# Kernel optimization log

Measured on AMD Instinct MI355X. Metric: run time of the kernel, lower is better.

The kernel has to match this reference:

```python
import jax, jax.numpy as jnp
import numpy as np

B, T, D = 4, 2048, 2048
N_HEADS, N_KV = 16, 4
HEAD_DIM = D // N_HEADS  # 128
N_REP = N_HEADS // N_KV
THETA = 10000.0


def _rope_cos_sin(seq_len, dim, theta):
    inv_freq = 1.0 / (theta ** (jnp.arange(0, dim, 2, dtype=jnp.float32) / dim))
    t = jnp.arange(seq_len, dtype=jnp.float32)
    freqs = jnp.outer(t, inv_freq)               # [T, dim/2]
    emb = jnp.concatenate([freqs, freqs], -1)    # [T, dim]
    return jnp.cos(emb)[None, None], jnp.sin(emb)[None, None]  # [1,1,T,dim]


def _rotate_half(x):
    x1, x2 = jnp.split(x, 2, axis=-1)
    return jnp.concatenate([-x2, x1], axis=-1)


def setup_inputs() -> dict:
    key = jax.random.key(0)
    ks = jax.random.split(key, 5)
    x = jax.random.normal(ks[0], (B, T, D), dtype=jnp.float32)
    # additive causal mask
    causal = jnp.tril(jnp.ones((T, T), dtype=bool))
    mask = jnp.where(causal, 0.0, -1e9).astype(jnp.float32)[None, None]
    s = 0.02
    wq = jax.random.normal(ks[1], (D, N_HEADS * HEAD_DIM), dtype=jnp.float32) * s
    wk = jax.random.normal(ks[2], (D, N_KV * HEAD_DIM), dtype=jnp.float32) * s
    wv = jax.random.normal(ks[3], (D, N_KV * HEAD_DIM), dtype=jnp.float32) * s
    wo = jax.random.normal(ks[4], (D, D), dtype=jnp.float32) * s
    return {"x": x, "mask": mask, "wq": wq, "wk": wk, "wv": wv, "wo": wo}


def reference(x, mask, wq, wk, wv, wo):
    Bc, Tc, _ = x.shape
    q = (x @ wq).reshape(Bc, Tc, N_HEADS, HEAD_DIM).transpose(0, 2, 1, 3)  # [B,H,T,hd]
    k = (x @ wk).reshape(Bc, Tc, N_KV, HEAD_DIM).transpose(0, 2, 1, 3)     # [B,Kv,T,hd]
    v = (x @ wv).reshape(Bc, Tc, N_KV, HEAD_DIM).transpose(0, 2, 1, 3)

    cos, sin = _rope_cos_sin(Tc, HEAD_DIM, THETA)
    q = q * cos + _rotate_half(q) * sin
    k = k * cos + _rotate_half(k) * sin

    # repeat kv heads: [B,Kv,T,hd] -> [B,Kv*n_rep,T,hd]
    k = jnp.repeat(k, N_REP, axis=1)
    v = jnp.repeat(v, N_REP, axis=1)

    scale = HEAD_DIM ** -0.5
    attn = jnp.einsum("bhqd,bhkd->bhqk", q, k) * scale
    attn = attn + mask
    attn = jax.nn.softmax(attn, axis=-1)
    out = jnp.einsum("bhqk,bhkd->bhqd", attn, v)  # [B,H,T,hd]
    out = out.transpose(0, 2, 1, 3).reshape(Bc, Tc, -1)
    return out @ wo
```

## Files before the change

kernel.cpp:

```cpp
#include <hip/hip_runtime.h>

typedef __bf16 bf16;
typedef float  f32x4  __attribute__((ext_vector_type(4)));
typedef float  f32x2  __attribute__((ext_vector_type(2)));
typedef float  f32x16 __attribute__((ext_vector_type(16)));
typedef __bf16 bf16x8 __attribute__((ext_vector_type(8)));
typedef __bf16 bf16x4 __attribute__((ext_vector_type(4)));
typedef unsigned short ushort4_ __attribute__((ext_vector_type(4)));
typedef unsigned int   uint2_   __attribute__((ext_vector_type(2)));

typedef unsigned int __attribute__((address_space(1))) uint_g;
typedef unsigned int __attribute__((address_space(3))) uint_l;

#define DEV __device__ __forceinline__

DEV void gload16(const void* g, void* l) {
  __builtin_amdgcn_global_load_lds((uint_g*)g, (uint_l*)l, 16, 0, 0);
}

#define PHASE_SYNC do { \
  asm volatile("s_barrier" ::: "memory"); \
  asm volatile("s_waitcnt lgkmcnt(0)" ::: "memory"); \
  __builtin_amdgcn_sched_barrier(0); } while (0)

__global__ void k_cvt(const float* __restrict__ in, bf16* __restrict__ out) {
  int i = blockIdx.x * 256 + threadIdx.x;
  f32x4 v = *((const f32x4*)in + i);
  bf16x4 o;
  o[0] = (bf16)v[0]; o[1] = (bf16)v[1]; o[2] = (bf16)v[2]; o[3] = (bf16)v[3];
  *((bf16x4*)out + i) = o;
}

__global__ void k_transpose_cvt(const float* __restrict__ in, bf16* __restrict__ out,
                                int K, int N) {
  __shared__ bf16 tile[64][65];
  int n0 = blockIdx.x * 64, k0 = blockIdx.y * 64;
  int tx = threadIdx.x & 63, ty = threadIdx.x >> 6;
#pragma unroll
  for (int r = 0; r < 64; r += 4)
    tile[r + ty][tx] = (bf16)in[(size_t)(k0 + r + ty) * N + n0 + tx];
  __syncthreads();
#pragma unroll
  for (int r = 0; r < 64; r += 4)
    out[(size_t)(n0 + r + ty) * K + k0 + tx] = tile[tx][r + ty];
}

__global__ void k_rope_tab(f32x2* __restrict__ tab) {
  int idx = blockIdx.x * 256 + threadIdx.x;
  int t = idx >> 6, i = idx & 63;
  float inv = powf(10000.f, -(float)i * (1.f / 64.f));
  float ang = (float)t * inv;
  f32x2 cs; cs[0] = cosf(ang); cs[1] = sinf(ang);
  tab[idx] = cs;
}

template <int MODE>
__global__ __launch_bounds__(512, 2) void k_gemm256(const bf16* __restrict__ A,
                                                    const bf16* __restrict__ Bt,
                                                    void* __restrict__ Cq,
                                                    bf16* __restrict__ Ck,
                                                    bf16* __restrict__ Cv,
                                                    int K) {
  __shared__ bf16 Asm[2][256 * 64];
  __shared__ bf16 Bsm[2][256 * 64];
  const int tid = threadIdx.x;
  const int w = tid >> 6, l = tid & 63, lr = l & 15, lg = l >> 4;
  const int wr = w >> 2, wc = w & 3;
  const int bn = blockIdx.x, bm = blockIdx.y;

  const int srow = tid >> 3;
  const int scb = ((tid & 7) << 4) ^ ((srow & 7) << 4);
  const bf16* Ag = A  + ((size_t)(bm * 256) + srow) * K;
  const bf16* Bg = Bt + ((size_t)(bn * 256) + srow) * K;
  const int ldsbase = w << 10;

  auto stA = [&](int buf, int s, int k0) {
    gload16((const char*)Ag + ((size_t)(s * 64) * K + k0) * 2 + scb,
            (char*)&Asm[buf][0] + s * 8192 + ldsbase);
  };
  auto stB = [&](int buf, int s, int k0) {
    gload16((const char*)Bg + ((size_t)(s * 64) * K + k0) * 2 + scb,
            (char*)&Bsm[buf][0] + s * 8192 + ldsbase);
  };
  auto ldA = [&](int buf, int mf, int kk) -> bf16x8 {
    int row = wr * 128 + mf * 16 + lr;
    return *(const bf16x8*)((const char*)&Asm[buf][0] + row * 128 +
                            ((kk * 64 + lg * 16) ^ ((lr & 7) << 4)));
  };
  auto ldB = [&](int buf, int nf, int kk) -> bf16x8 {
    int row = wc * 64 + nf * 16 + lr;
    return *(const bf16x8*)((const char*)&Bsm[buf][0] + row * 128 +
                            ((kk * 64 + lg * 16) ^ ((lr & 7) << 4)));
  };

  f32x4 acc[8][4] = {};
  const int nt = K >> 6;

#pragma unroll
  for (int s = 0; s < 4; s++) { stA(0, s, 0); stB(0, s, 0); }
  asm volatile("s_waitcnt vmcnt(0)" ::: "memory");
  __syncthreads();

#pragma unroll 1
  for (int t = 0; t < nt; t++) {
    const int cur = t & 1, nxt = cur ^ 1;
    const int kn = (t + 1) << 6;
    const bool pre = (t + 1 < nt);
    bf16x8 a0[4][2], a1[4][2], b0[2][2], b1[2][2];

#pragma unroll
    for (int mf = 0; mf < 4; mf++) { a0[mf][0] = ldA(cur, mf, 0); a0[mf][1] = ldA(cur, mf, 1); }
#pragma unroll
    for (int nf = 0; nf < 2; nf++) { b0[nf][0] = ldB(cur, nf, 0); b0[nf][1] = ldB(cur, nf, 1); }
    if (pre) { stA(nxt, 0, kn); stA(nxt, 1, kn); stA(nxt, 2, kn); }
    PHASE_SYNC;
    __builtin_amdgcn_s_setprio(1);
#pragma unroll
    for (int mf = 0; mf < 4; mf++)
#pragma unroll
      for (int nf = 0; nf < 2; nf++)
#pragma unroll
        for (int kk = 0; kk < 2; kk++)
          acc[mf][nf] = __builtin_amdgcn_mfma_f32_16x16x32_bf16(a0[mf][kk], b0[nf][kk], acc[mf][nf], 0, 0, 0);
    __builtin_amdgcn_s_setprio(0);

#pragma unroll
    for (int nf = 0; nf < 2; nf++) { b1[nf][0] = ldB(cur, nf + 2, 0); b1[nf][1] = ldB(cur, nf + 2, 1); }
    if (pre) { stA(nxt, 3, kn); stB(nxt, 0, kn); stB(nxt, 1, kn); }
    PHASE_SYNC;
    __builtin_amdgcn_s_setprio(1);
#pragma unroll
    for (int mf = 0; mf < 4; mf++)
#pragma unroll
      for (int nf = 0; nf < 2; nf++)
#pragma unroll
        for (int kk = 0; kk < 2; kk++)
          acc[mf][nf + 2] = __builtin_amdgcn_mfma_f32_16x16x32_bf16(a0[mf][kk], b1[nf][kk], acc[mf][nf + 2], 0, 0, 0);
    __builtin_amdgcn_s_setprio(0);

#pragma unroll
    for (int mf = 0; mf < 4; mf++) { a1[mf][0] = ldA(cur, mf + 4, 0); a1[mf][1] = ldA(cur, mf + 4, 1); }
#pragma unroll
    for (int nf = 0; nf < 2; nf++) { b0[nf][0] = ldB(cur, nf, 0); b0[nf][1] = ldB(cur, nf, 1); }
    if (pre) { stB(nxt, 2, kn); stB(nxt, 3, kn); }
    PHASE_SYNC;
    __builtin_amdgcn_s_setprio(1);
#pragma unroll
    for (int mf = 0; mf < 4; mf++)
#pragma unroll
      for (int nf = 0; nf < 2; nf++)
#pragma unroll
        for (int kk = 0; kk < 2; kk++)
          acc[mf + 4][nf] = __builtin_amdgcn_mfma_f32_16x16x32_bf16(a1[mf][kk], b0[nf][kk], acc[mf + 4][nf], 0, 0, 0);
    __builtin_amdgcn_s_setprio(0);

    __builtin_amdgcn_s_setprio(1);
#pragma unroll
    for (int mf = 0; mf < 4; mf++)
#pragma unroll
      for (int nf = 0; nf < 2; nf++)
#pragma unroll
        for (int kk = 0; kk < 2; kk++)
          acc[mf + 4][nf + 2] = __builtin_amdgcn_mfma_f32_16x16x32_bf16(a1[mf][kk], b1[nf][kk], acc[mf + 4][nf + 2], 0, 0, 0);
    __builtin_amdgcn_s_setprio(0);
    asm volatile("s_waitcnt vmcnt(0)" ::: "memory");
    asm volatile("s_barrier" ::: "memory");
  }

#pragma unroll
  for (int mf = 0; mf < 8; mf++) {
    const int rowb = bm * 256 + wr * 128 + mf * 16 + lg * 4;
#pragma unroll
    for (int nf = 0; nf < 4; nf++) {
      const int col = bn * 256 + wc * 64 + nf * 16 + lr;
      if constexpr (MODE == 0) {
        float* Cf = (float*)Cq;
#pragma unroll
        for (int j = 0; j < 4; j++)
          Cf[(size_t)(rowb + j) * 2048 + col] = acc[mf][nf][j];
      } else {
        if (bn < 8) {
          bf16* Cb = (bf16*)Cq;
#pragma unroll
          for (int j = 0; j < 4; j++)
            Cb[(size_t)(rowb + j) * 2048 + col] = (bf16)acc[mf][nf][j];
        } else if (bn < 10) {
          int kcol = col - 2048;
#pragma unroll
          for (int j = 0; j < 4; j++)
            Ck[(size_t)(rowb + j) * 512 + kcol] = (bf16)acc[mf][nf][j];
        } else {
          int vcol = col - 2560;
          int kv = vcol >> 7, d = vcol & 127;
          int bb = rowb >> 11, t0 = rowb & 2047;
          size_t off = ((size_t)((bb * 4 + kv) * 128 + d)) * 2048 + t0;
          ushort4_ pk;
#pragma unroll
          for (int j = 0; j < 4; j++)
            pk[j] = __builtin_bit_cast(unsigned short, (bf16)acc[mf][nf][j]);
          *(ushort4_*)(Cv + off) = pk;
        }
      }
    }
  }
}

template <int LOGNH>
__global__ void k_rope(const bf16* __restrict__ in, bf16* __restrict__ out,
                       const f32x2* __restrict__ tab, float scl) {
  const int NH = 1 << LOGNH;
  int idx = blockIdx.x * 256 + threadIdx.x;
  int dq = idx & 15;
  int h = (idx >> 4) & (NH - 1);
  int bt = idx >> (4 + LOGNH);
  int t = bt & 2047;
  int d0 = dq * 4;
  const bf16* pin = in + (size_t)bt * (NH * 128) + h * 128;
  bf16x4 x1 = *(const bf16x4*)(pin + d0);
  bf16x4 x2 = *(const bf16x4*)(pin + 64 + d0);
  bf16x4 o1, o2;
#pragma unroll
  for (int j = 0; j < 4; j++) {
    f32x2 cs = tab[t * 64 + d0 + j];
    float c1 = cs[0] * scl, s1 = cs[1] * scl;
    float a = (float)x1[j], c2 = (float)x2[j];
    o1[j] = (bf16)(a * c1 - c2 * s1);
    o2[j] = (bf16)(c2 * c1 + a * s1);
  }
  int b = bt >> 11;
  bf16* pout = out + (((size_t)(b << LOGNH) + h) * 2048 + t) * 128;
  *(bf16x4*)(pout + d0) = o1;
  *(bf16x4*)(pout + 64 + d0) = o2;
}

__global__ __launch_bounds__(256, 2) void k_attn(const bf16* __restrict__ Qb,
                                                 const bf16* __restrict__ Kb,
                                                 const bf16* __restrict__ Vt,
                                                 bf16* __restrict__ AO) {
  __shared__ bf16 Ks[2][64 * 128];
  __shared__ bf16 Vs[2][128 * 64];
  __shared__ bf16 Ps[4][32 * 64];
  const int tid = threadIdx.x, w = tid >> 6, l = tid & 63;
  const int bh = blockIdx.y, b = bh >> 4, h = bh & 15, kvh = h >> 2;
  const int pi = blockIdx.x;
  const int l31 = l & 31, hi = l >> 5;

  const bf16* Kh = Kb + (size_t)(b * 4 + kvh) * (2048 * 128);
  const bf16* Vh = Vt + (size_t)(b * 4 + kvh) * (128 * 2048);
  char* Pw = (char*)&Ps[w][0] + l31 * 128;
  const int qsw = (l & 7) << 4;

  auto stage = [&](int kv0, int buf) {
#pragma unroll
    for (int i = 0; i < 4; i++) {
      int krow = w * 16 + i * 4 + (l >> 4);
      int kcb = ((l & 15) * 16) ^ ((krow & 7) << 4);
      gload16(Kh + (size_t)(kv0 + krow) * 128 + (kcb >> 1), (bf16*)&Ks[buf][0] + w * 2048 + i * 512);
      int vrow = w * 32 + i * 8 + (l >> 3);
      int vcb = ((l & 7) * 16) ^ ((vrow & 7) << 4);
      gload16(Vh + (size_t)vrow * 2048 + kv0 + (vcb >> 1), (bf16*)&Vs[buf][0] + w * 2048 + i * 512);
    }
  };

#pragma unroll 1
  for (int ph = 0; ph < 2; ph++) {
    const int q0 = (ph ? (15 - pi) : pi) * 128;
    const int nt = q0 / 64 + 2;
    const int qw0 = q0 + w * 32;
    const int qg = qw0 + l31;

    bf16x8 qf[8];
    {
      const bf16* qp = Qb + (((size_t)(b * 16 + h) * 2048) + qg) * 128 + hi * 8;
#pragma unroll
      for (int kk = 0; kk < 8; kk++) qf[kk] = *(const bf16x8*)(qp + kk * 16);
    }

    f32x16 ot[4] = {};
    float m_ = -3e38f, l_ = 0.f;

    int cur = 0;
    stage(0, 0);
    __syncthreads();

#pragma unroll 1
    for (int t = 0; t < nt; t++) {
      const int kv0 = t * 64;
      if (t + 1 < nt) stage(kv0 + 64, cur ^ 1);

      if (kv0 <= qw0 + 31) {
        f32x16 st[2] = {};
        __builtin_amdgcn_s_setprio(1);
#pragma unroll
        for (int nb = 0; nb < 2; nb++) {
          const int row = nb * 32 + l31;
          const char* kbase = (const char*)&Ks[cur][0] + row * 256;
#pragma unroll
          for (int kk = 0; kk < 8; kk++) {
            bf16x8 kf = *(const bf16x8*)(kbase + ((kk * 32 + hi * 16) ^ qsw));
            st[nb] = __builtin_amdgcn_mfma_f32_32x32x16_bf16(kf, qf[kk], st[nb], 0, 0, 0);
          }
        }
        __builtin_amdgcn_s_setprio(0);

        if (kv0 + 63 > qw0) {
#pragma unroll
          for (int nb = 0; nb < 2; nb++) {
            const int kvb = kv0 + nb * 32 + 4 * hi;
#pragma unroll
            for (int r = 0; r < 16; r++) {
              int kg = kvb + (r & 3) + 8 * (r >> 2);
              if (kg > qg) st[nb][r] = -3e38f;
            }
          }
        }
        float mx = -3e38f;
#pragma unroll
        for (int nb = 0; nb < 2; nb++)
#pragma unroll
          for (int r = 0; r < 16; r++) mx = fmaxf(mx, st[nb][r]);
        mx = fmaxf(mx, __shfl_xor(mx, 32));
        if (!__all(mx - m_ <= 8.f)) {
          float mnew = fmaxf(m_, mx);
          float corr = exp2f(m_ - mnew);
          m_ = mnew; l_ *= corr;
#pragma unroll
          for (int dt = 0; dt < 4; dt++)
#pragma unroll
            for (int r = 0; r < 16; r++) ot[dt][r] *= corr;
        }
        float ls = 0.f;
#pragma unroll
        for (int nb = 0; nb < 2; nb++)
#pragma unroll
          for (int a = 0; a < 4; a++) {
            uint2_ pr;
#pragma unroll
            for (int half = 0; half < 2; half++) {
              float p0 = exp2f(st[nb][4 * a + 2 * half] - m_);
              float p1 = exp2f(st[nb][4 * a + 2 * half + 1] - m_);
              ls += p0 + p1;
              unsigned short b0 = __builtin_bit_cast(unsigned short, (bf16)p0);
              unsigned short b1 = __builtin_bit_cast(unsigned short, (bf16)p1);
              pr[half] = (unsigned int)b0 | ((unsigned int)b1 << 16);
            }
            *(uint2_*)(Pw + ((nb * 64 + a * 16 + hi * 8) ^ qsw)) = pr;
          }
        ls += __shfl_xor(ls, 32);
        l_ += ls;

        __builtin_amdgcn_s_setprio(1);
#pragma unroll
        for (int kb = 0; kb < 4; kb++) {
          bf16x8 pb = *(const bf16x8*)(Pw + ((kb * 32 + hi * 16) ^ qsw));
#pragma unroll
          for (int dt = 0; dt < 4; dt++) {
            const int vrow = dt * 32 + l31;
            const char* vp = (const char*)&Vs[cur][0] + vrow * 128 + ((kb * 32 + hi * 16) ^ qsw);
            bf16x8 vf = *(const bf16x8*)vp;
            ot[dt] = __builtin_amdgcn_mfma_f32_32x32x16_bf16(vf, pb, ot[dt], 0, 0, 0);
          }
        }
        __builtin_amdgcn_s_setprio(0);
      }

      __syncthreads();
      cur ^= 1;
    }

    const float inv = 1.f / l_;
    bf16* op = AO + ((size_t)b * 2048 + qg) * 2048 + h * 128;
#pragma unroll
    for (int dt = 0; dt < 4; dt++)
#pragma unroll
      for (int rq = 0; rq < 4; rq++) {
        ushort4_ pk;
#pragma unroll
        for (int j = 0; j < 4; j++)
          pk[j] = __builtin_bit_cast(unsigned short, (bf16)(ot[dt][rq * 4 + j] * inv));
        *(ushort4_*)(op + dt * 32 + rq * 8 + hi * 4) = pk;
      }
  }
}

extern "C" void kernel_launch(void* const* d_in, const int* in_sizes, int n_in,
                              void* d_out, int out_size, void* d_ws, size_t ws_size,
                              hipStream_t stream) {
  const float* x  = (const float*)d_in[0];
  const float* wq = (const float*)d_in[2];
  const float* wk = (const float*)d_in[3];
  const float* wv = (const float*)d_in[4];
  const float* wo = (const float*)d_in[5];

  char* p = (char*)d_ws;
  auto alloc = [&](size_t bytes) { char* r = p; p += (bytes + 255) & ~(size_t)255; return r; };
  bf16*  xb     = (bf16*)alloc(8192ull * 2048 * 2);
  bf16*  wqkvT  = (bf16*)alloc(3072ull * 2048 * 2);
  bf16*  woT    = (bf16*)alloc(2048ull * 2048 * 2);
  f32x2* tab    = (f32x2*)alloc(2048ull * 64 * 8);
  bf16*  Qtmp   = (bf16*)alloc(8192ull * 2048 * 2);
  bf16*  Ktmp   = (bf16*)alloc(8192ull * 512 * 2);
  bf16*  Qr     = (bf16*)alloc(8192ull * 2048 * 2);
  bf16*  Kr     = (bf16*)alloc(8192ull * 512 * 2);
  bf16*  Vr     = (bf16*)alloc(8192ull * 512 * 2);

  k_cvt<<<16384, 256, 0, stream>>>(x, xb);
  k_transpose_cvt<<<dim3(32, 32), 256, 0, stream>>>(wq, wqkvT, 2048, 2048);
  k_transpose_cvt<<<dim3(8, 32),  256, 0, stream>>>(wk, wqkvT + 2048ull * 2048, 2048, 512);
  k_transpose_cvt<<<dim3(8, 32),  256, 0, stream>>>(wv, wqkvT + 2560ull * 2048, 2048, 512);
  k_transpose_cvt<<<dim3(32, 32), 256, 0, stream>>>(wo, woT, 2048, 2048);
  k_rope_tab<<<512, 256, 0, stream>>>(tab);

  k_gemm256<1><<<dim3(12, 32), 512, 0, stream>>>(xb, wqkvT, Qtmp, Ktmp, Vr, 2048);

  const float qscl = 0.08838834764831845f * 1.4426950408889634f;
  k_rope<4><<<8192, 256, 0, stream>>>(Qtmp, Qr, tab, qscl);
  k_rope<2><<<2048, 256, 0, stream>>>(Ktmp, Kr, tab, 1.0f);

  k_attn<<<dim3(8, 64), 256, 0, stream>>>(Qr, Kr, Vr, Qtmp);

  k_gemm256<0><<<dim3(8, 32), 512, 0, stream>>>(Qtmp, woT, d_out, nullptr, nullptr, 2048);
}
```

Baseline: 349.4 us.

## Reorder GEMM prefetch stages with finer barriers and partial vmcnt waits

Reworks the double-buffered bf16 GEMM main loop so the next tile's B stages are issued first and the A stages are spread across later phases. Each MFMA block now gets its own s_barrier, and the end-of-iteration full vmcnt(0) drain becomes partial vmcnt waits so some global-to-LDS loads stay in flight. The explicit lgkmcnt waits and sched_barrier are dropped, and launch bounds go from two blocks per CU to one, which frees registers. The risk is a hazard: if a read of the current buffer depends on an A stage still covered by a partial wait, results could be wrong, and the extra barriers add sync cost.

```diff
diff --git a/kernel.cpp b/kernel.cpp
--- a/kernel.cpp
+++ b/kernel.cpp
@@ -18,10 +18,8 @@
   __builtin_amdgcn_global_load_lds((uint_g*)g, (uint_l*)l, 16, 0, 0);
 }
 
-#define PHASE_SYNC do { \
-  asm volatile("s_barrier" ::: "memory"); \
-  asm volatile("s_waitcnt lgkmcnt(0)" ::: "memory"); \
-  __builtin_amdgcn_sched_barrier(0); } while (0)
+#define SBAR  asm volatile("s_barrier" ::: "memory")
+#define VMCNT(n) asm volatile("s_waitcnt vmcnt(" #n ")" ::: "memory")
 
 __global__ void k_cvt(const float* __restrict__ in, bf16* __restrict__ out) {
   int i = blockIdx.x * 256 + threadIdx.x;
@@ -55,7 +53,7 @@
 }
 
 template <int MODE>
-__global__ __launch_bounds__(512, 2) void k_gemm256(const bf16* __restrict__ A,
+__global__ __launch_bounds__(512, 1) void k_gemm256(const bf16* __restrict__ A,
                                                     const bf16* __restrict__ Bt,
                                                     void* __restrict__ Cq,
                                                     bf16* __restrict__ Ck,
@@ -98,8 +96,8 @@
 
 #pragma unroll
   for (int s = 0; s < 4; s++) { stA(0, s, 0); stB(0, s, 0); }
-  asm volatile("s_waitcnt vmcnt(0)" ::: "memory");
-  __syncthreads();
+  VMCNT(0);
+  SBAR;
 
 #pragma unroll 1
   for (int t = 0; t < nt; t++) {
@@ -112,8 +110,8 @@
     for (int mf = 0; mf < 4; mf++) { a0[mf][0] = ldA(cur, mf, 0); a0[mf][1] = ldA(cur, mf, 1); }
 #pragma unroll
     for (int nf = 0; nf < 2; nf++) { b0[nf][0] = ldB(cur, nf, 0); b0[nf][1] = ldB(cur, nf, 1); }
-    if (pre) { stA(nxt, 0, kn); stA(nxt, 1, kn); stA(nxt, 2, kn); }
-    PHASE_SYNC;
+    if (pre) { stB(nxt, 0, kn); stB(nxt, 1, kn); }
+    SBAR;
     __builtin_amdgcn_s_setprio(1);
 #pragma unroll
     for (int mf = 0; mf < 4; mf++)
@@ -123,11 +121,12 @@
         for (int kk = 0; kk < 2; kk++)
           acc[mf][nf] = __builtin_amdgcn_mfma_f32_16x16x32_bf16(a0[mf][kk], b0[nf][kk], acc[mf][nf], 0, 0, 0);
     __builtin_amdgcn_s_setprio(0);
+    SBAR;
 
 #pragma unroll
     for (int nf = 0; nf < 2; nf++) { b1[nf][0] = ldB(cur, nf + 2, 0); b1[nf][1] = ldB(cur, nf + 2, 1); }
-    if (pre) { stA(nxt, 3, kn); stB(nxt, 0, kn); stB(nxt, 1, kn); }
-    PHASE_SYNC;
+    if (pre) { stB(nxt, 2, kn); stB(nxt, 3, kn); }
+    SBAR;
     __builtin_amdgcn_s_setprio(1);
 #pragma unroll
     for (int mf = 0; mf < 4; mf++)
@@ -137,13 +136,15 @@
         for (int kk = 0; kk < 2; kk++)
           acc[mf][nf + 2] = __builtin_amdgcn_mfma_f32_16x16x32_bf16(a0[mf][kk], b1[nf][kk], acc[mf][nf + 2], 0, 0, 0);
     __builtin_amdgcn_s_setprio(0);
+    VMCNT(4);
+    SBAR;
 
 #pragma unroll
     for (int mf = 0; mf < 4; mf++) { a1[mf][0] = ldA(cur, mf + 4, 0); a1[mf][1] = ldA(cur, mf + 4, 1); }
 #pragma unroll
     for (int nf = 0; nf < 2; nf++) { b0[nf][0] = ldB(cur, nf, 0); b0[nf][1] = ldB(cur, nf, 1); }
-    if (pre) { stB(nxt, 2, kn); stB(nxt, 3, kn); }
-    PHASE_SYNC;
+    if (pre) { stA(nxt, 0, kn); stA(nxt, 2, kn); }
+    SBAR;
     __builtin_amdgcn_s_setprio(1);
 #pragma unroll
     for (int mf = 0; mf < 4; mf++)
@@ -153,7 +154,10 @@
         for (int kk = 0; kk < 2; kk++)
           acc[mf + 4][nf] = __builtin_amdgcn_mfma_f32_16x16x32_bf16(a1[mf][kk], b0[nf][kk], acc[mf + 4][nf], 0, 0, 0);
     __builtin_amdgcn_s_setprio(0);
-
+    SBAR;
+
+    if (pre) { stA(nxt, 1, kn); stA(nxt, 3, kn); }
+    SBAR;
     __builtin_amdgcn_s_setprio(1);
 #pragma unroll
     for (int mf = 0; mf < 4; mf++)
@@ -163,8 +167,8 @@
         for (int kk = 0; kk < 2; kk++)
           acc[mf + 4][nf + 2] = __builtin_amdgcn_mfma_f32_16x16x32_bf16(a1[mf][kk], b1[nf][kk], acc[mf + 4][nf + 2], 0, 0, 0);
     __builtin_amdgcn_s_setprio(0);
-    asm volatile("s_waitcnt vmcnt(0)" ::: "memory");
-    asm volatile("s_barrier" ::: "memory");
+    VMCNT(2);
+    SBAR;
   }
 
 #pragma unroll
```

Measured after the change: 358.8 us. 1.03x slower.
